# Kernel tuning notes

Measured on AMD Instinct MI355X. Metric: run time of the kernel, lower is better.

Reference implementation:

```python
import jax, jax.numpy as jnp
import numpy as np

N, E, G = 50000, 800000, 64
IN, HID, H, OUT = 128, 64, 4, 10


def _gat_layer(x, src, dst, W, a_src, a_dst, b):
    # x: [N, Fin]; W: [H*C, Fin]; a_src/a_dst: [H, C]; b: [H*C]
    n = x.shape[0]
    C = a_src.shape[1]
    h = (x @ W.T).reshape(n, H, C)                      # [N, H, C]
    e_src = jnp.einsum('nhc,hc->nh', h, a_src)          # [N, H]
    e_dst = jnp.einsum('nhc,hc->nh', h, a_dst)          # [N, H]
    logits = jax.nn.leaky_relu(e_src[src] + e_dst[dst], 0.2)  # [E', H]
    # segment softmax over destination node
    m = jax.ops.segment_max(logits, dst, num_segments=n)
    ex = jnp.exp(logits - m[dst])
    denom = jax.ops.segment_sum(ex, dst, num_segments=n)
    alpha = ex / (denom[dst] + 1e-16)                   # [E', H]
    msg = h[src] * alpha[:, :, None]                    # [E', H, C]
    out = jax.ops.segment_sum(msg, dst, num_segments=n) # [N, H, C]
    return out.reshape(n, H * C) + b


def setup_inputs() -> dict:
    key = jax.random.key(0)
    ks = jax.random.split(key, 20)
    x = jax.random.normal(ks[0], (N, IN), dtype=jnp.float32)
    edge_index = jax.random.randint(ks[1], (2, E), 0, N, dtype=jnp.int64)
    batch = jnp.sort(jax.random.randint(ks[2], (N,), 0, G, dtype=jnp.int64))

    def glorot(k, shape):
        fan = shape[-1]
        return jax.random.normal(k, shape, dtype=jnp.float32) / jnp.sqrt(jnp.float32(fan))

    ins = [IN, HID * H, HID * H]
    params = {}
    for i, fin in enumerate(ins, start=1):
        params[f'W{i}'] = glorot(ks[3 * i], (H * HID, fin))
        params[f'a_src{i}'] = glorot(ks[3 * i + 1], (H, HID))
        params[f'a_dst{i}'] = glorot(ks[3 * i + 2], (H, HID))
        params[f'b{i}'] = jnp.zeros((H * HID,), dtype=jnp.float32)
    params['Wl'] = glorot(ks[13], (OUT, H * HID))
    params['bl'] = jnp.zeros((OUT,), dtype=jnp.float32)
    return dict(x=x, edge_index=edge_index, batch=batch, **params)


def reference(x, edge_index, batch,
              W1, a_src1, a_dst1, b1,
              W2, a_src2, a_dst2, b2,
              W3, a_src3, a_dst3, b3,
              Wl, bl):
    n = x.shape[0]
    loops = jnp.arange(n, dtype=edge_index.dtype)
    src = jnp.concatenate([edge_index[0], loops])  # add self-loops (PyG default)
    dst = jnp.concatenate([edge_index[1], loops])

    h = jax.nn.elu(_gat_layer(x, src, dst, W1, a_src1, a_dst1, b1))
    h = jax.nn.elu(_gat_layer(h, src, dst, W2, a_src2, a_dst2, b2))
    h = _gat_layer(h, src, dst, W3, a_src3, a_dst3, b3)

    # global mean pool over graphs
    sums = jax.ops.segment_sum(h, batch, num_segments=G)          # [G, H*HID]
    counts = jax.ops.segment_sum(jnp.ones((n,), h.dtype), batch, num_segments=G)
    pooled = sums / jnp.maximum(counts, 1.0)[:, None]
    return pooled @ Wl.T + bl                                      # [G, OUT]
```

## Files before the change

kernel.cpp:

```cpp
#include <hip/hip_runtime.h>
#include <hip/hip_bf16.h>
#include <math.h>

#define NNODES 50000
#define NEDGES 800000
#define NGRAPH 64
#define FIN 128
#define HC 256
#define NHEAD 4
#define NOUT 10
#define ETOT (NEDGES + NNODES)
#define NB196 ((NNODES + 255) / 256)
#define BCAP 5376
#define S1CHUNK 4096
#define NBS1 ((ETOT + S1CHUNK - 1) / S1CHUNK)


typedef unsigned short u16;
typedef unsigned char u8;
typedef __attribute__((ext_vector_type(8))) short short8;
typedef __attribute__((ext_vector_type(4))) float f32x4;
typedef __attribute__((ext_vector_type(2))) float f32x2;

__device__ inline u16 f2b(float f) {
    union { float f; unsigned u; } v; v.f = f;
    unsigned r = v.u + 0x7FFF + ((v.u >> 16) & 1);
    return (u16)(r >> 16);
}
__device__ inline float b2f(u16 u) {
    union { unsigned u; float f; } v; v.u = ((unsigned)u) << 16; return v.f;
}

__device__ inline void gload_lds16(const void* g, void* l) {
    __builtin_amdgcn_global_load_lds(
        (const __attribute__((address_space(1))) unsigned*)g,
        (__attribute__((address_space(3))) unsigned*)l, 16, 0, 0);
}

__device__ inline int lbound(const int* __restrict__ batch, int g) {
    int lo = 0, hi = NNODES;
    while (lo < hi) {
        int mid = (lo + hi) >> 1;
        if (batch[mid] < g) lo = mid + 1; else hi = mid;
    }
    return lo;
}


#define CS0 (NNODES * FIN)
#define CS1 (HC * FIN)
#define CS2 (HC * HC)
#define NBCONV (((CS0 + CS1 + 2 * CS2) / 4 + 255) / 256)

__global__ __launch_bounds__(256) void prep_kernel(const float* __restrict__ x,
                                                   const float* __restrict__ W1,
                                                   const float* __restrict__ W2,
                                                   const float* __restrict__ W3,
                                                   u16* __restrict__ xb, u16* __restrict__ w1b,
                                                   u16* __restrict__ w2b, u16* __restrict__ w3b,
                                                   const int* __restrict__ ei,
                                                   int* __restrict__ bcur,
                                                   unsigned* __restrict__ tmp) {
    __shared__ int hist[NB196];
    __shared__ int basec[NB196];
    int b = blockIdx.x;
    if (b < NBCONV) {
        long i = (long)(b * 256 + threadIdx.x) * 4;
        if (i < CS0) {
            float4 v = *(const float4*)(x + i);
            ushort4 o;
            o.x = f2b(v.x); o.y = f2b(v.y); o.z = f2b(v.z); o.w = f2b(v.w);
            *(ushort4*)(xb + i) = o;
        } else if (i < CS0 + CS1) {
            long off = i - CS0;
            float4 v = *(const float4*)(W1 + off);
            ushort4 o;
            o.x = f2b(v.x); o.y = f2b(v.y); o.z = f2b(v.z); o.w = f2b(v.w);
            *(ushort4*)(w1b + off) = o;
        } else if (i < CS0 + CS1 + 2 * CS2) {
            const float* src; u16* dst; long off;
            if (i < CS0 + CS1 + CS2) { src = W2; dst = w2b; off = i - CS0 - CS1; }
            else                     { src = W3; dst = w3b; off = i - CS0 - CS1 - CS2; }
            float4 v = *(const float4*)(src + off);
            int row = (int)(off >> 8), col = (int)(off & 255);
            float vv[4] = {v.x, v.y, v.z, v.w};
            #pragma unroll
            for (int k = 0; k < 4; ++k) {
                int c = col + k;
                int pp = (c & ~63) | ((c & 15) << 2) | ((c >> 4) & 3);
                dst[row * 256 + pp] = f2b(vv[k]);
            }
        }
        return;
    }
    int tid = threadIdx.x;
    int e0 = (b - NBCONV) * S1CHUNK;
    for (int i = tid; i < NB196; i += 256) hist[i] = 0;
    __syncthreads();
    int bkt[16], rnk[16];
    unsigned pk[16];
    #pragma unroll
    for (int k = 0; k < 16; ++k) {
        int e = e0 + k * 256 + tid;
        bkt[k] = -1;
        if (e < ETOT) {
            int src, dstn;
            if (e < NEDGES) { src = ei[e]; dstn = ei[NEDGES + e]; }
            else            { src = dstn = e - NEDGES; }
            int bb = dstn >> 8;
            bkt[k] = bb;
            rnk[k] = atomicAdd(&hist[bb], 1);
            pk[k] = (unsigned)src | ((unsigned)(dstn & 255) << 16);
        }
    }
    __syncthreads();
    for (int i = tid; i < NB196; i += 256) {
        int h = hist[i];
        basec[i] = h ? atomicAdd(&bcur[i], h) : 0;
    }
    __syncthreads();
    #pragma unroll
    for (int k = 0; k < 16; ++k) {
        if (bkt[k] >= 0) {
            int pos = basec[bkt[k]] + rnk[k];
            if (pos < BCAP)
                tmp[(size_t)bkt[k] * BCAP + pos] = pk[k];
        }
    }
}


__global__ __launch_bounds__(256) void scatter2_kernel(const unsigned* __restrict__ tmp,
                                                       const int* __restrict__ bcur,
                                                       int* __restrict__ off,
                                                       int* __restrict__ ssrc) {
    __shared__ unsigned ebuf[BCAP];
    __shared__ int ldss[BCAP];
    __shared__ int cnt[256];
    __shared__ int loff[256];
    __shared__ int ws[4];
    __shared__ int sbase;
    int b = blockIdx.x;
    int tid = threadIdx.x;
    int lane = tid & 63, wid = tid >> 6;

    int bv = 0;
    if (tid < NB196) { bv = bcur[tid]; if (bv > BCAP) bv = BCAP; }
    {
        int x = bv;
        #pragma unroll
        for (int o = 1; o < 64; o <<= 1) {
            int t = __shfl_up(x, o);
            if (lane >= o) x += t;
        }
        if (lane == 63) ws[wid] = x;
        __syncthreads();
        if (tid < 4) {
            int w = ws[tid];
            #pragma unroll
            for (int o = 1; o < 4; o <<= 1) {
                int t = __shfl_up(w, o, 4);
                if ((tid & 3) >= o) w += t;
            }
            ws[tid] = w;
        }
        __syncthreads();
        int wexcl = wid ? ws[wid - 1] : 0;
        int gexcl = x - bv + wexcl;
        if (tid == b) sbase = gexcl;
        __syncthreads();
    }
    int s = sbase;
    int n = bcur[b];
    if (n > BCAP) n = BCAP;

    cnt[tid] = 0;
    const unsigned* tb = tmp + (size_t)b * BCAP;
    for (int i = tid; i < n; i += 256) ebuf[i] = tb[i];
    __syncthreads();
    for (int i = tid; i < n; i += 256) atomicAdd(&cnt[ebuf[i] >> 16], 1);
    __syncthreads();
    int v = cnt[tid];
    int x = v;
    #pragma unroll
    for (int o = 1; o < 64; o <<= 1) {
        int t = __shfl_up(x, o);
        if (lane >= o) x += t;
    }
    if (lane == 63) ws[wid] = x;
    __syncthreads();
    if (tid < 4) {
        int w = ws[tid];
        #pragma unroll
        for (int o = 1; o < 4; o <<= 1) {
            int t = __shfl_up(w, o, 4);
            if ((tid & 3) >= o) w += t;
        }
        ws[tid] = w;
    }
    __syncthreads();
    int wexcl = wid ? ws[wid - 1] : 0;
    int excl = x - v + wexcl;
    loff[tid] = excl;
    off[b * 256 + tid] = s + excl;
    cnt[tid] = 0;
    __syncthreads();
    for (int i = tid; i < n; i += 256) {
        unsigned pk = ebuf[i];
        int ld = (int)(pk >> 16);
        int rank = atomicAdd(&cnt[ld], 1);
        ldss[loff[ld] + rank] = (int)(pk & 0xFFFFu);
    }
    __syncthreads();
    for (int i = tid; i < n; i += 256) ssrc[s + i] = ldss[i];
}


#define TBM 128
#define TBN 128
#define TBK 32

__global__ __launch_bounds__(256) void gemm_mfma(const u16* __restrict__ A,
                                                 const u16* __restrict__ B,
                                                 u8* __restrict__ C, int K,
                                                 const float* __restrict__ asrc,
                                                 const float* __restrict__ adst,
                                                 float* __restrict__ es,
                                                 float* __restrict__ ed) {
    __shared__ u16 Als[TBM * TBK];
    __shared__ u16 Bls[TBN * TBK];
    int tid = threadIdx.x;
    int wave = tid >> 6, lane = tid & 63;
    int brow = blockIdx.x * TBM, bcol = blockIdx.y * TBN;
    int m_base = (wave >> 1) * 64, n_base = (wave & 1) * 64;
    int r0 = tid >> 2, kc = (tid & 3) * 8;
    int lquad = lane >> 4, l16 = lane & 15;

    f32x4 acc[4][4] = {};

    const u16* ga0 = A + (size_t)(brow + r0) * K + kc;
    const u16* ga1 = A + (size_t)(brow + 64 + r0) * K + kc;
    const u16* gb0 = B + (size_t)(bcol + r0) * K + kc;
    const u16* gb1 = B + (size_t)(bcol + 64 + r0) * K + kc;
    u16* la0 = &Als[r0 * TBK + kc];
    u16* la1 = &Als[(64 + r0) * TBK + kc];
    u16* lb0 = &Bls[r0 * TBK + kc];
    u16* lb1 = &Bls[(64 + r0) * TBK + kc];

    for (int k0 = 0; k0 < K; k0 += TBK) {
        __syncthreads();
        gload_lds16(ga0 + k0, la0);
        gload_lds16(ga1 + k0, la1);
        gload_lds16(gb0 + k0, lb0);
        gload_lds16(gb1 + k0, lb1);
        __syncthreads();
        short8 fa[4], fb[4];
        #pragma unroll
        for (int i = 0; i < 4; ++i) {
            fa[i] = *(const short8*)(&Als[(m_base + i * 16 + l16) * TBK + lquad * 8]);
            fb[i] = *(const short8*)(&Bls[(n_base + i * 16 + l16) * TBK + lquad * 8]);
        }
        #pragma unroll
        for (int i = 0; i < 4; ++i)
            #pragma unroll
            for (int j = 0; j < 4; ++j)
                acc[i][j] = __builtin_amdgcn_mfma_f32_16x16x32_bf16(fa[i], fb[j], acc[i][j], 0, 0, 0);
    }

    #pragma unroll
    for (int i = 0; i < 4; ++i) {
        int rbase = brow + m_base + i * 16 + lquad * 4;
        #pragma unroll
        for (int r = 0; r < 4; ++r) {
            int row = rbase + r;
            if (row < NNODES) {
                int u = 0;
                u = __builtin_amdgcn_cvt_pk_fp8_f32(acc[i][0][r], acc[i][1][r], u, false);
                u = __builtin_amdgcn_cvt_pk_fp8_f32(acc[i][2][r], acc[i][3][r], u, true);
                *(int*)(C + (size_t)row * HC + bcol + n_base + l16 * 4) = u;
            }
        }
    }

    int head = (bcol + n_base) >> 6;
    float asv[4], adv[4];
    #pragma unroll
    for (int j = 0; j < 4; ++j) {
        asv[j] = asrc[head * 64 + j * 16 + l16];
        adv[j] = adst[head * 64 + j * 16 + l16];
    }
    #pragma unroll
    for (int i = 0; i < 4; ++i) {
        #pragma unroll
        for (int r = 0; r < 4; ++r) {
            float ps = 0.f, pd = 0.f;
            #pragma unroll
            for (int j = 0; j < 4; ++j) {
                ps = fmaf(acc[i][j][r], asv[j], ps);
                pd = fmaf(acc[i][j][r], adv[j], pd);
            }
            #pragma unroll
            for (int o = 1; o < 16; o <<= 1) {
                ps += __shfl_xor(ps, o);
                pd += __shfl_xor(pd, o);
            }
            int row = brow + m_base + i * 16 + lquad * 4 + r;
            if (l16 == 0 && row < NNODES) {
                es[row * 4 + head] = ps;
                ed[row * 4 + head] = pd;
            }
        }
    }
}


__global__ __launch_bounds__(256) void aggregate_kernel(const u8* __restrict__ h,
                                                        const int* __restrict__ ssrc,
                                                        const int* __restrict__ off,
                                                        const float* __restrict__ es,
                                                        const float* __restrict__ ed,
                                                        const float* __restrict__ bias,
                                                        u16* __restrict__ out,
                                                        int apply_elu) {
    __shared__ int2 xch[4][4][17];
    const unsigned* h32 = (const unsigned*)h;
    int wid = threadIdx.x >> 6;
    int dst = blockIdx.x * 4 + wid;
    if (dst >= NNODES) return;
    int lane = threadIdx.x & 63;
    int head = lane >> 4;
    int j16 = lane & 15;
    int s = off[dst];
    int e = off[dst + 1];
    float edh = ed[dst * 4 + head];
    int2* myslot = &xch[wid][head][0];

    float a0 = 0.f, a1 = 0.f, a2 = 0.f, a3 = 0.f, dpriv = 0.f;

    int base = s;
    for (; base + 16 <= e; base += 16) {
        int mysrc = ssrc[base + j16];
        float l = es[mysrc * 4 + head] + edh;
        l = fmaxf(l, 0.2f * l);
        float myex = __expf(l);
        dpriv += myex;
        myslot[j16] = make_int2(mysrc, __float_as_int(myex));
        #pragma unroll
        for (int j = 0; j < 16; ++j) {
            int2 pr = myslot[j];
            float exj = __int_as_float(pr.y);
            unsigned hv = h32[(unsigned)pr.x * 64 + lane];
            f32x2 lo = __builtin_amdgcn_cvt_pk_f32_fp8(hv, false);
            f32x2 hi = __builtin_amdgcn_cvt_pk_f32_fp8(hv, true);
            a0 += lo.x * exj;
            a1 += lo.y * exj;
            a2 += hi.x * exj;
            a3 += hi.y * exj;
        }
    }
    int cnt = e - base;
    if (cnt > 0) {
        int mysrc = 0; float myex = 0.f;
        if (j16 < cnt) {
            mysrc = ssrc[base + j16];
            float l = es[mysrc * 4 + head] + edh;
            l = fmaxf(l, 0.2f * l);
            myex = __expf(l);
            dpriv += myex;
        }
        myslot[j16] = make_int2(mysrc, __float_as_int(myex));
        for (int j = 0; j < cnt; ++j) {
            int2 pr = myslot[j];
            float exj = __int_as_float(pr.y);
            unsigned hv = h32[(unsigned)pr.x * 64 + lane];
            f32x2 lo = __builtin_amdgcn_cvt_pk_f32_fp8(hv, false);
            f32x2 hi = __builtin_amdgcn_cvt_pk_f32_fp8(hv, true);
            a0 += lo.x * exj;
            a1 += lo.y * exj;
            a2 += hi.x * exj;
            a3 += hi.y * exj;
        }
    }
    #pragma unroll
    for (int o = 1; o < 16; o <<= 1) dpriv += __shfl_xor(dpriv, o);
    float inv = 1.f / (dpriv + 1e-16f);
    int bbase = ((lane >> 4) << 6) | (lane & 15);
    float b0 = bias[bbase], b1 = bias[bbase + 16], b2 = bias[bbase + 32], b3 = bias[bbase + 48];
    float o0 = a0 * inv + b0;
    float o1 = a1 * inv + b1;
    float o2 = a2 * inv + b2;
    float o3 = a3 * inv + b3;
    if (apply_elu) {
        o0 = o0 > 0.f ? o0 : __expf(o0) - 1.f;
        o1 = o1 > 0.f ? o1 : __expf(o1) - 1.f;
        o2 = o2 > 0.f ? o2 : __expf(o2) - 1.f;
        o3 = o3 > 0.f ? o3 : __expf(o3) - 1.f;
    }
    ushort4 ov;
    ov.x = f2b(o0); ov.y = f2b(o1); ov.z = f2b(o2); ov.w = f2b(o3);
    *(ushort4*)(out + (size_t)dst * HC + lane * 4) = ov;
}


__global__ __launch_bounds__(256) void pool_kernel(const u16* __restrict__ hin,
                                                   const int* __restrict__ batch,
                                                   float* __restrict__ pp) {
    int g = blockIdx.x;
    int slice = blockIdx.y;
    int lane = threadIdx.x & 63;
    int wid = threadIdx.x >> 6;
    int s = lbound(batch, g), e = lbound(batch, g + 1);
    float a0 = 0.f, a1 = 0.f, a2 = 0.f, a3 = 0.f;
    for (int n = s + slice * 4 + wid; n < e; n += 32) {
        ushort4 hv = *(const ushort4*)(hin + (size_t)n * HC + lane * 4);
        a0 += b2f(hv.x); a1 += b2f(hv.y); a2 += b2f(hv.z); a3 += b2f(hv.w);
    }
    __shared__ float4 part[4][64];
    part[wid][lane] = make_float4(a0, a1, a2, a3);
    __syncthreads();
    if (wid == 0) {
        float4 p0 = part[0][lane], p1 = part[1][lane], p2 = part[2][lane], p3 = part[3][lane];
        float4 v = make_float4((p0.x + p1.x) + (p2.x + p3.x),
                               (p0.y + p1.y) + (p2.y + p3.y),
                               (p0.z + p1.z) + (p2.z + p3.z),
                               (p0.w + p1.w) + (p2.w + p3.w));
        *(float4*)(pp + ((size_t)(g * 8 + slice)) * HC + lane * 4) = v;
    }
}


__global__ __launch_bounds__(64) void final_kernel(const float* __restrict__ pp,
                                                   const int* __restrict__ batch,
                                                   const float* __restrict__ Wl,
                                                   const float* __restrict__ bl,
                                                   float* __restrict__ out) {
    int g = blockIdx.x;
    int lane = threadIdx.x;
    float4 pv = make_float4(0.f, 0.f, 0.f, 0.f);
    #pragma unroll
    for (int sl = 0; sl < 8; ++sl) {
        float4 v = *(const float4*)(pp + ((size_t)(g * 8 + sl)) * HC + lane * 4);
        pv.x += v.x; pv.y += v.y; pv.z += v.z; pv.w += v.w;
    }
    int cs = lbound(batch, g), ce = lbound(batch, g + 1);
    float cntf = fmaxf((float)(ce - cs), 1.f);
    float inv = 1.f / cntf;
    pv.x *= inv; pv.y *= inv; pv.z *= inv; pv.w *= inv;
    int wbase = ((lane >> 4) << 6) | (lane & 15);
    float acc[NOUT];
    #pragma unroll
    for (int o = 0; o < NOUT; ++o) {
        const float* w = Wl + o * HC + wbase;
        acc[o] = pv.x * w[0] + pv.y * w[16] + pv.z * w[32] + pv.w * w[48];
    }
    #pragma unroll
    for (int s = 32; s > 0; s >>= 1)
        #pragma unroll
        for (int o = 0; o < NOUT; ++o)
            acc[o] += __shfl_xor(acc[o], s);
    if (lane == 0) {
        #pragma unroll
        for (int o = 0; o < NOUT; ++o)
            out[g * NOUT + o] = acc[o] + bl[o];
    }
}


extern "C" void kernel_launch(void* const* d_in, const int* in_sizes, int n_in,
                              void* d_out, int out_size, void* d_ws, size_t ws_size,
                              hipStream_t stream) {
    (void)in_sizes; (void)n_in; (void)out_size; (void)ws_size;
    const float* x   = (const float*)d_in[0];
    const int*   ei  = (const int*)d_in[1];
    const int*   bat = (const int*)d_in[2];
    const float* W1  = (const float*)d_in[3];
    const float* as1 = (const float*)d_in[4];
    const float* ad1 = (const float*)d_in[5];
    const float* b1  = (const float*)d_in[6];
    const float* W2  = (const float*)d_in[7];
    const float* as2 = (const float*)d_in[8];
    const float* ad2 = (const float*)d_in[9];
    const float* b2  = (const float*)d_in[10];
    const float* W3  = (const float*)d_in[11];
    const float* as3 = (const float*)d_in[12];
    const float* ad3 = (const float*)d_in[13];
    const float* b3  = (const float*)d_in[14];
    const float* Wl  = (const float*)d_in[15];
    const float* bl  = (const float*)d_in[16];
    float* out = (float*)d_out;

    char* ws = (char*)d_ws;
    size_t p = 0;
    auto alloc = [&](size_t bytes) {
        size_t a = p;
        p += (bytes + 255) & ~(size_t)255;
        return a;
    };
    int*      off  = (int*)(ws + alloc((size_t)(NB196 * 256 + 256) * 4));
    int*      bcur = (int*)(ws + alloc(256 * 4));
    int*      ssrc = (int*)(ws + alloc((size_t)ETOT * 4));
    unsigned* tmp  = (unsigned*)(ws + alloc((size_t)NB196 * BCAP * 4));
    float*    es   = (float*)(ws + alloc((size_t)NNODES * NHEAD * 4));
    float*    ed   = (float*)(ws + alloc((size_t)NNODES * NHEAD * 4));
    u16*      xb   = (u16*)(ws + alloc((size_t)NNODES * FIN * 2));
    u16*      w1b  = (u16*)(ws + alloc((size_t)HC * FIN * 2));
    u16*      w2b  = (u16*)(ws + alloc((size_t)HC * HC * 2));
    u16*      w3b  = (u16*)(ws + alloc((size_t)HC * HC * 2));
    u8*       Hb   = (u8*)(ws + alloc((size_t)NNODES * HC));
    u16*      Ab   = (u16*)(ws + alloc((size_t)NNODES * HC * 2));
    float*    pp   = (float*)(ws + alloc((size_t)NGRAPH * 8 * HC * 4));
    alloc(128 * 1024);

    hipMemsetAsync(bcur, 0, 256 * 4, stream);

    prep_kernel<<<NBCONV + NBS1, 256, 0, stream>>>(x, W1, W2, W3, xb, w1b, w2b, w3b,
                                                   ei, bcur, tmp);
    scatter2_kernel<<<NB196, 256, 0, stream>>>(tmp, bcur, off, ssrc);

    dim3 ggrid((NNODES + TBM - 1) / TBM, HC / TBN);
    int nblocks4 = (NNODES + 3) / 4;

    gemm_mfma<<<ggrid, 256, 0, stream>>>(xb, w1b, Hb, FIN, as1, ad1, es, ed);
    aggregate_kernel<<<nblocks4, 256, 0, stream>>>(Hb, ssrc, off, es, ed, b1, Ab, 1);
    gemm_mfma<<<ggrid, 256, 0, stream>>>(Ab, w2b, Hb, HC, as2, ad2, es, ed);
    aggregate_kernel<<<nblocks4, 256, 0, stream>>>(Hb, ssrc, off, es, ed, b2, Ab, 1);
    gemm_mfma<<<ggrid, 256, 0, stream>>>(Ab, w3b, Hb, HC, as3, ad3, es, ed);
    aggregate_kernel<<<nblocks4, 256, 0, stream>>>(Hb, ssrc, off, es, ed, b3, Ab, 0);

    dim3 pgrid(NGRAPH, 8);
    pool_kernel<<<pgrid, 256, 0, stream>>>(Ab, bat, pp);
    final_kernel<<<NGRAPH, 64, 0, stream>>>(pp, bat, Wl, bl, out);
}
```

Measured before the change: 342.9 us.

## Double GEMM K-tile to 64 with XOR-swizzled LDS layout

```diff
diff --git a/kernel.cpp b/kernel.cpp
--- a/kernel.cpp
+++ b/kernel.cpp
@@ -218,7 +218,7 @@
 
 #define TBM 128
 #define TBN 128
-#define TBK 32
+#define TBK 64
 
 __global__ __launch_bounds__(256) void gemm_mfma(const u16* __restrict__ A,
                                                  const u16* __restrict__ B,
@@ -233,38 +233,44 @@
     int wave = tid >> 6, lane = tid & 63;
     int brow = blockIdx.x * TBM, bcol = blockIdx.y * TBN;
     int m_base = (wave >> 1) * 64, n_base = (wave & 1) * 64;
-    int r0 = tid >> 2, kc = (tid & 3) * 8;
     int lquad = lane >> 4, l16 = lane & 15;
 
+    int r_loc = tid >> 3;
+    int sc    = tid & 7;
+    int kcs   = (sc ^ (r_loc & 7)) * 8;
+
     f32x4 acc[4][4] = {};
 
-    const u16* ga0 = A + (size_t)(brow + r0) * K + kc;
-    const u16* ga1 = A + (size_t)(brow + 64 + r0) * K + kc;
-    const u16* gb0 = B + (size_t)(bcol + r0) * K + kc;
-    const u16* gb1 = B + (size_t)(bcol + 64 + r0) * K + kc;
-    u16* la0 = &Als[r0 * TBK + kc];
-    u16* la1 = &Als[(64 + r0) * TBK + kc];
-    u16* lb0 = &Bls[r0 * TBK + kc];
-    u16* lb1 = &Bls[(64 + r0) * TBK + kc];
+    const u16* gaBase = A + (size_t)(brow + r_loc) * K + kcs;
+    const u16* gbBase = B + (size_t)(bcol + r_loc) * K + kcs;
+    u16* laBase = &Als[tid * 8];
+    u16* lbBase = &Bls[tid * 8];
 
     for (int k0 = 0; k0 < K; k0 += TBK) {
         __syncthreads();
-        gload_lds16(ga0 + k0, la0);
-        gload_lds16(ga1 + k0, la1);
-        gload_lds16(gb0 + k0, lb0);
-        gload_lds16(gb1 + k0, lb1);
+        #pragma unroll
+        for (int q = 0; q < 4; ++q) {
+            gload_lds16(gaBase + (size_t)(q * 32) * K + k0, laBase + q * 2048);
+            gload_lds16(gbBase + (size_t)(q * 32) * K + k0, lbBase + q * 2048);
+        }
         __syncthreads();
-        short8 fa[4], fb[4];
-        #pragma unroll
-        for (int i = 0; i < 4; ++i) {
-            fa[i] = *(const short8*)(&Als[(m_base + i * 16 + l16) * TBK + lquad * 8]);
-            fb[i] = *(const short8*)(&Bls[(n_base + i * 16 + l16) * TBK + lquad * 8]);
-        }
-        #pragma unroll
-        for (int i = 0; i < 4; ++i)
+        #pragma unroll
+        for (int kh = 0; kh < 2; ++kh) {
+            short8 fa[4], fb[4];
+            int ca = kh * 4 + lquad;
             #pragma unroll
-            for (int j = 0; j < 4; ++j)
-                acc[i][j] = __builtin_amdgcn_mfma_f32_16x16x32_bf16(fa[i], fb[j], acc[i][j], 0, 0, 0);
+            for (int i = 0; i < 4; ++i) {
+                int Ra = m_base + i * 16 + l16;
+                int Rb = n_base + i * 16 + l16;
+                fa[i] = *(const short8*)(&Als[Ra * 64 + ((ca ^ (Ra & 7)) * 8)]);
+                fb[i] = *(const short8*)(&Bls[Rb * 64 + ((ca ^ (Rb & 7)) * 8)]);
+            }
+            #pragma unroll
+            for (int i = 0; i < 4; ++i)
+                #pragma unroll
+                for (int j = 0; j < 4; ++j)
+                    acc[i][j] = __builtin_amdgcn_mfma_f32_16x16x32_bf16(fa[i], fb[j], acc[i][j], 0, 0, 0);
+        }
     }
 
     #pragma unroll
```

Result: no change. 339.1 us (median of 2 runs) (-1.1%).
